# Kernel optimization log

Hardware: AMD Instinct MI355X
Metric: run time of the kernel (lower is better)

The kernel has to match this reference:

```python
import jax, jax.numpy as jnp
import numpy as np
import math

B, NB, HID, KD, NH = 256, 16, 512, 64, 8

def setup_inputs() -> dict:
    key = jax.random.key(0)
    ks = jax.random.split(key, 6)
    s = lambda fan_in: 1.0 / math.sqrt(fan_in)
    return {
        "h": jax.random.normal(ks[0], (B, NB, HID), dtype=jnp.float32),
        "mask": jax.random.randint(ks[1], (B, NB), 0, 2, dtype=jnp.int32),
        "Wk": jax.random.normal(ks[2], (NB, HID, KD * NH), dtype=jnp.float32) * s(HID),
        "Wq": jax.random.normal(ks[3], (NB, HID, KD * NH), dtype=jnp.float32) * s(HID),
        "Wv": jax.random.normal(ks[4], (NB, HID, HID * NH), dtype=jnp.float32) * s(HID),
        "Wo": jax.random.normal(ks[5], (NB, HID * NH, HID), dtype=jnp.float32) * s(HID * NH),
    }

def _group_linear(x, w):
    # x: (B, NB, din), w: (NB, din, dout) -> (B, NB, dout)
    return jnp.einsum('bnd,nde->bne', x, w)

def reference(h, mask, Wk, Wq, Wv, Wo):
    # grouped QKV projections
    k = _group_linear(h, Wk).reshape(B, NB, NH, KD).transpose(0, 2, 1, 3)    # (B,H,NB,KD)
    q = _group_linear(h, Wq).reshape(B, NB, NH, KD).transpose(0, 2, 1, 3)    # (B,H,NB,KD)
    v = _group_linear(h, Wv).reshape(B, NB, NH, HID).transpose(0, 2, 1, 3)   # (B,H,NB,HID)
    scores = jnp.einsum('bhqd,bhkd->bhqk', q, k) / math.sqrt(KD)             # (B,H,NB,NB)
    probs = jax.nn.softmax(scores, axis=-1)
    # post-softmax row mask: mask (B,NB) -> (B,1,NB,1)
    probs = probs * mask.astype(probs.dtype)[:, None, :, None]
    ctx = jnp.einsum('bhqk,bhkd->bhqd', probs, v)                            # (B,H,NB,HID)
    ctx = ctx.transpose(0, 2, 1, 3).reshape(B, NB, NH * HID)                 # (B,NB,H*HID)
    return _group_linear(ctx, Wo)                                            # (B,NB,HID)
```

## Files before the change

kernel.cpp:

```cpp
#include <hip/hip_runtime.h>


typedef short s16x4 __attribute__((ext_vector_type(4)));
typedef short s16x8 __attribute__((ext_vector_type(8)));
typedef float f32x4 __attribute__((ext_vector_type(4)));

__device__ __forceinline__ unsigned short f2bf(float f) {
  unsigned int u = __builtin_bit_cast(unsigned int, f);
  u += 0x7fffu + ((u >> 16) & 1u);
  return (unsigned short)(u >> 16);
}
__device__ __forceinline__ float bf2f(unsigned short s) {
  unsigned int u = ((unsigned int)s) << 16;
  return __builtin_bit_cast(float, u);
}

__global__ __launch_bounds__(256) void qkv_gemm(
    const float* __restrict__ h, const float* __restrict__ Wq,
    const float* __restrict__ Wk, const float* __restrict__ Wv,
    unsigned short* __restrict__ qo, unsigned short* __restrict__ ko,
    unsigned short* __restrict__ vo)
{
  const int g    = blockIdx.y;
  const int m0   = (blockIdx.x / 40) * 128;
  const int n0   = (blockIdx.x % 40) * 128;
  const int tid  = threadIdx.x;
  const int lane = tid & 63;
  const int wave = tid >> 6;
  const int wm   = (wave >> 1) * 64;
  const int wn   = (wave & 1) * 64;

  const float* W; unsigned short* out; int obase, oldc, wN, c0;
  if (n0 < 512)       { W = Wq + (size_t)g * 262144;  out = qo; obase = g * 512;  oldc = 8192;  wN = 512;  c0 = n0; }
  else if (n0 < 1024) { W = Wk + (size_t)g * 262144;  out = ko; obase = g * 512;  oldc = 8192;  wN = 512;  c0 = n0 - 512; }
  else                { W = Wv + (size_t)g * 2097152; out = vo; obase = g * 4096; oldc = 65536; wN = 4096; c0 = n0 - 1024; }

  const float* A = h + (size_t)g * 512 + (size_t)m0 * 8192;

  __shared__ unsigned short As[128][32];
  __shared__ unsigned short Bs[128][36];

  f32x4 acc[4][4];
  #pragma unroll
  for (int i = 0; i < 4; i++)
    #pragma unroll
    for (int j = 0; j < 4; j++) acc[i][j] = (f32x4){0.f, 0.f, 0.f, 0.f};

  const int fr = lane & 15, fq = lane >> 4;

  for (int k0 = 0; k0 < 512; k0 += 32) {
    __syncthreads();
    #pragma unroll
    for (int p = 0; p < 4; p++) {
      int idx = p * 256 + tid;
      int row = idx >> 3, kc = idx & 7;
      float4 av = *reinterpret_cast<const float4*>(A + (size_t)row * 8192 + k0 + kc * 4);
      s16x4 st = { (short)f2bf(av.x), (short)f2bf(av.y), (short)f2bf(av.z), (short)f2bf(av.w) };
      *reinterpret_cast<s16x4*>(&As[row][kc * 4]) = st;
    }
    #pragma unroll
    for (int p = 0; p < 4; p++) {
      int idx = p * 256 + tid;
      int n = idx & 127, kc = idx >> 7;
      const float* wp = W + (size_t)(k0 + kc * 4) * wN + c0 + n;
      float w0 = wp[0], w1 = wp[wN], w2 = wp[2 * wN], w3 = wp[3 * wN];
      s16x4 st = { (short)f2bf(w0), (short)f2bf(w1), (short)f2bf(w2), (short)f2bf(w3) };
      *reinterpret_cast<s16x4*>(&Bs[n][kc * 4]) = st;
    }
    __syncthreads();
    s16x8 af[4], bfr[4];
    #pragma unroll
    for (int mi = 0; mi < 4; mi++)
      af[mi] = *reinterpret_cast<const s16x8*>(&As[wm + mi * 16 + fr][fq * 8]);
    #pragma unroll
    for (int ni = 0; ni < 4; ni++) {
      const s16x4* bp = reinterpret_cast<const s16x4*>(&Bs[wn + ni * 16 + fr][fq * 8]);
      s16x4 lo = bp[0], hi = bp[1];
      bfr[ni] = __builtin_shufflevector(lo, hi, 0, 1, 2, 3, 4, 5, 6, 7);
    }
    #pragma unroll
    for (int mi = 0; mi < 4; mi++)
      #pragma unroll
      for (int ni = 0; ni < 4; ni++)
        acc[mi][ni] = __builtin_amdgcn_mfma_f32_16x16x32_bf16(af[mi], bfr[ni], acc[mi][ni], 0, 0, 0);
  }

  #pragma unroll
  for (int mi = 0; mi < 4; mi++)
    #pragma unroll
    for (int ni = 0; ni < 4; ni++)
      #pragma unroll
      for (int r = 0; r < 4; r++) {
        int row = m0 + wm + mi * 16 + fq * 4 + r;
        int col = c0 + wn + ni * 16 + fr;
        out[(size_t)obase + (size_t)row * oldc + col] = f2bf(acc[mi][ni][r]);
      }
}

__global__ __launch_bounds__(256) void attn_kernel(
    const unsigned short* __restrict__ q, const unsigned short* __restrict__ k,
    const unsigned short* __restrict__ v, const int* __restrict__ mask,
    unsigned short* __restrict__ ctx)
{
  const int b  = blockIdx.x >> 3;
  const int hh = blockIdx.x & 7;
  const int tid = threadIdx.x;

  __shared__ float qs[16][65];
  __shared__ float ks[16][65];
  __shared__ float sc[16][16];

  #pragma unroll
  for (int p = 0; p < 4; p++) {
    int idx = p * 256 + tid;
    int n = idx >> 6, d = idx & 63;
    size_t gi = ((size_t)(b * 16 + n) << 9) + (hh << 6) + d;
    qs[n][d] = bf2f(q[gi]);
    ks[n][d] = bf2f(k[gi]);
  }
  __syncthreads();
  {
    int qi = tid >> 4, ki = tid & 15;
    float s = 0.f;
    #pragma unroll
    for (int j = 0; j < 64; j++) s += qs[qi][j] * ks[ki][j];
    sc[qi][ki] = s * 0.125f;
  }
  __syncthreads();
  if (tid < 16) {
    float m = sc[tid][0];
    #pragma unroll
    for (int j = 1; j < 16; j++) m = fmaxf(m, sc[tid][j]);
    float ev[16], sum = 0.f;
    #pragma unroll
    for (int j = 0; j < 16; j++) { ev[j] = __expf(sc[tid][j] - m); sum += ev[j]; }
    float scale = (mask[b * 16 + tid] != 0) ? (1.f / sum) : 0.f;
    #pragma unroll
    for (int j = 0; j < 16; j++) sc[tid][j] = ev[j] * scale;
  }
  __syncthreads();
  #pragma unroll
  for (int p = 0; p < 2; p++) {
    int e0 = p * 256 + tid;
    float vv[16];
    #pragma unroll
    for (int kk = 0; kk < 16; kk++)
      vv[kk] = bf2f(v[((size_t)(b * 16 + kk) << 12) + (hh << 9) + e0]);
    #pragma unroll
    for (int qi = 0; qi < 16; qi++) {
      float s = 0.f;
      #pragma unroll
      for (int kk = 0; kk < 16; kk++) s += sc[qi][kk] * vv[kk];
      ctx[((size_t)(b * 16 + qi) << 12) + (hh << 9) + e0] = f2bf(s);
    }
  }
}

__global__ __launch_bounds__(256) void out_gemm(
    const unsigned short* __restrict__ ctxp, const float* __restrict__ Wo,
    float* __restrict__ outp)
{
  const int g    = blockIdx.y;
  const int bx   = blockIdx.x;
  const int sk   = bx >> 3;
  const int m0   = ((bx >> 2) & 1) * 128;
  const int n0   = (bx & 3) * 128;
  const int tid  = threadIdx.x;
  const int lane = tid & 63;
  const int wave = tid >> 6;
  const int wm   = (wave >> 1) * 64;
  const int wn   = (wave & 1) * 64;

  const unsigned short* A = ctxp + (size_t)g * 4096 + (size_t)m0 * 65536;
  const float* W = Wo + (size_t)g * 2097152;

  __shared__ unsigned short As[128][32];
  __shared__ unsigned short Bs[128][36];

  f32x4 acc[4][4];
  #pragma unroll
  for (int i = 0; i < 4; i++)
    #pragma unroll
    for (int j = 0; j < 4; j++) acc[i][j] = (f32x4){0.f, 0.f, 0.f, 0.f};

  const int fr = lane & 15, fq = lane >> 4;
  const int kend = sk * 2048 + 2048;

  for (int k0 = sk * 2048; k0 < kend; k0 += 32) {
    __syncthreads();
    #pragma unroll
    for (int p = 0; p < 4; p++) {
      int idx = p * 256 + tid;
      int row = idx >> 3, kc = idx & 7;
      s16x4 av = *reinterpret_cast<const s16x4*>(A + (size_t)row * 65536 + k0 + kc * 4);
      *reinterpret_cast<s16x4*>(&As[row][kc * 4]) = av;
    }
    #pragma unroll
    for (int p = 0; p < 4; p++) {
      int idx = p * 256 + tid;
      int n = idx & 127, kc = idx >> 7;
      const float* wp = W + (size_t)(k0 + kc * 4) * 512 + n0 + n;
      float w0 = wp[0], w1 = wp[512], w2 = wp[1024], w3 = wp[1536];
      s16x4 st = { (short)f2bf(w0), (short)f2bf(w1), (short)f2bf(w2), (short)f2bf(w3) };
      *reinterpret_cast<s16x4*>(&Bs[n][kc * 4]) = st;
    }
    __syncthreads();
    s16x8 af[4], bfr[4];
    #pragma unroll
    for (int mi = 0; mi < 4; mi++)
      af[mi] = *reinterpret_cast<const s16x8*>(&As[wm + mi * 16 + fr][fq * 8]);
    #pragma unroll
    for (int ni = 0; ni < 4; ni++) {
      const s16x4* bp = reinterpret_cast<const s16x4*>(&Bs[wn + ni * 16 + fr][fq * 8]);
      s16x4 lo = bp[0], hi = bp[1];
      bfr[ni] = __builtin_shufflevector(lo, hi, 0, 1, 2, 3, 4, 5, 6, 7);
    }
    #pragma unroll
    for (int mi = 0; mi < 4; mi++)
      #pragma unroll
      for (int ni = 0; ni < 4; ni++)
        acc[mi][ni] = __builtin_amdgcn_mfma_f32_16x16x32_bf16(af[mi], bfr[ni], acc[mi][ni], 0, 0, 0);
  }

  float* og = outp + (size_t)g * 512;
  #pragma unroll
  for (int mi = 0; mi < 4; mi++)
    #pragma unroll
    for (int ni = 0; ni < 4; ni++)
      #pragma unroll
      for (int r = 0; r < 4; r++) {
        int row = m0 + wm + mi * 16 + fq * 4 + r;
        int col = n0 + wn + ni * 16 + fr;
        atomicAdd(&og[(size_t)row * 8192 + col], acc[mi][ni][r]);
      }
}

extern "C" void kernel_launch(void* const* d_in, const int* in_sizes, int n_in,
                              void* d_out, int out_size, void* d_ws, size_t ws_size,
                              hipStream_t stream) {
  const float* h  = (const float*)d_in[0];
  const int* mask = (const int*)d_in[1];
  const float* Wk = (const float*)d_in[2];
  const float* Wq = (const float*)d_in[3];
  const float* Wv = (const float*)d_in[4];
  const float* Wo = (const float*)d_in[5];
  float* out = (float*)d_out;

  unsigned short* qws   = (unsigned short*)d_ws;
  unsigned short* kws   = qws + 2097152;
  unsigned short* vws   = kws + 2097152;
  unsigned short* ctxws = vws + 16777216;

  hipMemsetAsync(d_out, 0, (size_t)out_size * sizeof(float), stream);
  qkv_gemm<<<dim3(80, 16), 256, 0, stream>>>(h, Wq, Wk, Wv, qws, kws, vws);
  attn_kernel<<<2048, 256, 0, stream>>>(qws, kws, vws, mask, ctxws);
  out_gemm<<<dim3(16, 16), 256, 0, stream>>>(ctxws, Wo, out);
}
```

Baseline: 418.6 us.

## Retile GEMMs over full batch, pre-convert h, and replace atomics with split-K reduce

Adds a pass that converts h to bf16 once, so the QKV GEMM loads 16-byte bf16 A tiles. The QKV GEMM is retiled to 256x64, so each block covers the whole batch and each weight tile is read and converted only once. The attention kernel now uses vectorized ushort4 loads and stores, and each thread computes 8 query rows by 4 columns. The output GEMM uses 512-thread blocks with a 4-way split-K that writes partial sums to workspace, followed by a reduce kernel. This removes the memset and the float atomics, at the cost of extra partial-buffer traffic and two more launches.

```diff
diff --git a/kernel.cpp b/kernel.cpp
--- a/kernel.cpp
+++ b/kernel.cpp
@@ -15,202 +15,214 @@
   return __builtin_bit_cast(float, u);
 }
 
+__global__ __launch_bounds__(256) void cvt_h(const float* __restrict__ h,
+                                             unsigned short* __restrict__ hb)
+{
+  int i = (blockIdx.x * 256 + threadIdx.x) * 4;
+  float4 v = *reinterpret_cast<const float4*>(h + i);
+  s16x4 st = { (short)f2bf(v.x), (short)f2bf(v.y), (short)f2bf(v.z), (short)f2bf(v.w) };
+  *reinterpret_cast<s16x4*>(hb + i) = st;
+}
+
 __global__ __launch_bounds__(256) void qkv_gemm(
-    const float* __restrict__ h, const float* __restrict__ Wq,
+    const unsigned short* __restrict__ hb, const float* __restrict__ Wq,
     const float* __restrict__ Wk, const float* __restrict__ Wv,
     unsigned short* __restrict__ qo, unsigned short* __restrict__ ko,
     unsigned short* __restrict__ vo)
 {
   const int g    = blockIdx.y;
-  const int m0   = (blockIdx.x / 40) * 128;
-  const int n0   = (blockIdx.x % 40) * 128;
+  const int n0   = blockIdx.x * 64;
+  const int tid  = threadIdx.x;
+  const int lane = tid & 63;
+  const int wave = tid >> 6;
+  const int wm   = wave * 64;
+
+  const float* W; unsigned short* out; size_t obase; int oldc, wN, c0;
+  if (n0 < 512)       { W = Wq + (size_t)g * 262144;  out = qo; obase = (size_t)g * 512;  oldc = 8192;  wN = 512;  c0 = n0; }
+  else if (n0 < 1024) { W = Wk + (size_t)g * 262144;  out = ko; obase = (size_t)g * 512;  oldc = 8192;  wN = 512;  c0 = n0 - 512; }
+  else                { W = Wv + (size_t)g * 2097152; out = vo; obase = (size_t)g * 4096; oldc = 65536; wN = 4096; c0 = n0 - 1024; }
+
+  const unsigned short* A = hb + (size_t)g * 512;
+
+  __shared__ unsigned short As[256][32];
+  __shared__ unsigned short Bs[64][36];
+
+  f32x4 acc[4][4];
+  #pragma unroll
+  for (int i = 0; i < 4; i++)
+    #pragma unroll
+    for (int j = 0; j < 4; j++) acc[i][j] = (f32x4){0.f, 0.f, 0.f, 0.f};
+
+  const int fr = lane & 15, fq = lane >> 4;
+
+  for (int k0 = 0; k0 < 512; k0 += 32) {
+    __syncthreads();
+    #pragma unroll
+    for (int p = 0; p < 4; p++) {
+      int idx = p * 256 + tid;
+      int row = idx >> 2, kq = idx & 3;
+      *reinterpret_cast<s16x8*>(&As[row][kq * 8]) =
+          *reinterpret_cast<const s16x8*>(A + (size_t)row * 8192 + k0 + kq * 8);
+    }
+    #pragma unroll
+    for (int p = 0; p < 2; p++) {
+      int idx = p * 256 + tid;
+      int n = idx & 63, kc = idx >> 6;
+      const float* wp = W + (size_t)(k0 + kc * 4) * wN + c0 + n;
+      float w0 = wp[0], w1 = wp[wN], w2 = wp[2 * wN], w3 = wp[3 * wN];
+      s16x4 st = { (short)f2bf(w0), (short)f2bf(w1), (short)f2bf(w2), (short)f2bf(w3) };
+      *reinterpret_cast<s16x4*>(&Bs[n][kc * 4]) = st;
+    }
+    __syncthreads();
+    s16x8 af[4], bfr[4];
+    #pragma unroll
+    for (int mi = 0; mi < 4; mi++)
+      af[mi] = *reinterpret_cast<const s16x8*>(&As[wm + mi * 16 + fr][fq * 8]);
+    #pragma unroll
+    for (int ni = 0; ni < 4; ni++) {
+      const s16x4* bp = reinterpret_cast<const s16x4*>(&Bs[ni * 16 + fr][fq * 8]);
+      s16x4 lo = bp[0], hi = bp[1];
+      bfr[ni] = __builtin_shufflevector(lo, hi, 0, 1, 2, 3, 4, 5, 6, 7);
+    }
+    #pragma unroll
+    for (int mi = 0; mi < 4; mi++)
+      #pragma unroll
+      for (int ni = 0; ni < 4; ni++)
+        acc[mi][ni] = __builtin_amdgcn_mfma_f32_16x16x32_bf16(af[mi], bfr[ni], acc[mi][ni], 0, 0, 0);
+  }
+
+  #pragma unroll
+  for (int mi = 0; mi < 4; mi++)
+    #pragma unroll
+    for (int ni = 0; ni < 4; ni++)
+      #pragma unroll
+      for (int r = 0; r < 4; r++) {
+        int row = wm + mi * 16 + fq * 4 + r;
+        int col = c0 + ni * 16 + fr;
+        out[obase + (size_t)row * oldc + col] = f2bf(acc[mi][ni][r]);
+      }
+}
+
+__global__ __launch_bounds__(256) void attn_kernel(
+    const unsigned short* __restrict__ q, const unsigned short* __restrict__ k,
+    const unsigned short* __restrict__ v, const int* __restrict__ mask,
+    unsigned short* __restrict__ ctx)
+{
+  const int b  = blockIdx.x >> 3;
+  const int hh = blockIdx.x & 7;
+  const int tid = threadIdx.x;
+
+  __shared__ float qs[16][65];
+  __shared__ float ks[16][65];
+  __shared__ float sc[16][16];
+
+  {
+    int n = tid >> 4, d4 = (tid & 15) * 4;
+    size_t gi = ((size_t)(b * 16 + n) << 9) + (hh << 6) + d4;
+    ushort4 qv = *reinterpret_cast<const ushort4*>(q + gi);
+    ushort4 kv = *reinterpret_cast<const ushort4*>(k + gi);
+    qs[n][d4] = bf2f(qv.x); qs[n][d4+1] = bf2f(qv.y); qs[n][d4+2] = bf2f(qv.z); qs[n][d4+3] = bf2f(qv.w);
+    ks[n][d4] = bf2f(kv.x); ks[n][d4+1] = bf2f(kv.y); ks[n][d4+2] = bf2f(kv.z); ks[n][d4+3] = bf2f(kv.w);
+  }
+  __syncthreads();
+  {
+    int qi = tid >> 4, ki = tid & 15;
+    float s = 0.f;
+    #pragma unroll
+    for (int j = 0; j < 64; j++) s += qs[qi][j] * ks[ki][j];
+    sc[qi][ki] = s * 0.125f;
+  }
+  __syncthreads();
+  if (tid < 16) {
+    float m = sc[tid][0];
+    #pragma unroll
+    for (int j = 1; j < 16; j++) m = fmaxf(m, sc[tid][j]);
+    float ev[16], sum = 0.f;
+    #pragma unroll
+    for (int j = 0; j < 16; j++) { ev[j] = __expf(sc[tid][j] - m); sum += ev[j]; }
+    float scale = (mask[b * 16 + tid] != 0) ? (1.f / sum) : 0.f;
+    #pragma unroll
+    for (int j = 0; j < 16; j++) sc[tid][j] = ev[j] * scale;
+  }
+  __syncthreads();
+  {
+    int col4  = (tid & 127) * 4;
+    int qbase = (tid >> 7) * 8;
+    float a0[8], a1[8], a2[8], a3[8];
+    #pragma unroll
+    for (int j = 0; j < 8; j++) { a0[j] = 0.f; a1[j] = 0.f; a2[j] = 0.f; a3[j] = 0.f; }
+    #pragma unroll
+    for (int kk = 0; kk < 16; kk++) {
+      ushort4 vv = *reinterpret_cast<const ushort4*>(
+          v + ((size_t)(b * 16 + kk) << 12) + (hh << 9) + col4);
+      float v0 = bf2f(vv.x), v1 = bf2f(vv.y), v2 = bf2f(vv.z), v3 = bf2f(vv.w);
+      #pragma unroll
+      for (int j = 0; j < 8; j++) {
+        float p = sc[qbase + j][kk];
+        a0[j] += p * v0; a1[j] += p * v1; a2[j] += p * v2; a3[j] += p * v3;
+      }
+    }
+    #pragma unroll
+    for (int j = 0; j < 8; j++) {
+      ushort4 st = { f2bf(a0[j]), f2bf(a1[j]), f2bf(a2[j]), f2bf(a3[j]) };
+      *reinterpret_cast<ushort4*>(
+          ctx + ((size_t)(b * 16 + qbase + j) << 12) + (hh << 9) + col4) = st;
+    }
+  }
+}
+
+__global__ __launch_bounds__(512) void out_gemm(
+    const unsigned short* __restrict__ ctxp, const float* __restrict__ Wo,
+    float* __restrict__ partial)
+{
+  const int g    = blockIdx.y;
+  const int bx   = blockIdx.x;
+  const int sk   = bx >> 3;
+  const int n0   = (bx & 7) * 64;
   const int tid  = threadIdx.x;
   const int lane = tid & 63;
   const int wave = tid >> 6;
   const int wm   = (wave >> 1) * 64;
-  const int wn   = (wave & 1) * 64;
-
-  const float* W; unsigned short* out; int obase, oldc, wN, c0;
-  if (n0 < 512)       { W = Wq + (size_t)g * 262144;  out = qo; obase = g * 512;  oldc = 8192;  wN = 512;  c0 = n0; }
-  else if (n0 < 1024) { W = Wk + (size_t)g * 262144;  out = ko; obase = g * 512;  oldc = 8192;  wN = 512;  c0 = n0 - 512; }
-  else                { W = Wv + (size_t)g * 2097152; out = vo; obase = g * 4096; oldc = 65536; wN = 4096; c0 = n0 - 1024; }
-
-  const float* A = h + (size_t)g * 512 + (size_t)m0 * 8192;
-
-  __shared__ unsigned short As[128][32];
-  __shared__ unsigned short Bs[128][36];
-
-  f32x4 acc[4][4];
+  const int wn   = (wave & 1) * 32;
+
+  const unsigned short* A = ctxp + (size_t)g * 4096;
+  const float* W = Wo + (size_t)g * 2097152;
+
+  __shared__ unsigned short As[256][32];
+  __shared__ unsigned short Bs[64][36];
+
+  f32x4 acc[4][2];
   #pragma unroll
   for (int i = 0; i < 4; i++)
     #pragma unroll
-    for (int j = 0; j < 4; j++) acc[i][j] = (f32x4){0.f, 0.f, 0.f, 0.f};
+    for (int j = 0; j < 2; j++) acc[i][j] = (f32x4){0.f, 0.f, 0.f, 0.f};
 
   const int fr = lane & 15, fq = lane >> 4;
-
-  for (int k0 = 0; k0 < 512; k0 += 32) {
-    __syncthreads();
-    #pragma unroll
-    for (int p = 0; p < 4; p++) {
-      int idx = p * 256 + tid;
-      int row = idx >> 3, kc = idx & 7;
-      float4 av = *reinterpret_cast<const float4*>(A + (size_t)row * 8192 + k0 + kc * 4);
-      s16x4 st = { (short)f2bf(av.x), (short)f2bf(av.y), (short)f2bf(av.z), (short)f2bf(av.w) };
-      *reinterpret_cast<s16x4*>(&As[row][kc * 4]) = st;
-    }
-    #pragma unroll
-    for (int p = 0; p < 4; p++) {
-      int idx = p * 256 + tid;
-      int n = idx & 127, kc = idx >> 7;
-      const float* wp = W + (size_t)(k0 + kc * 4) * wN + c0 + n;
-      float w0 = wp[0], w1 = wp[wN], w2 = wp[2 * wN], w3 = wp[3 * wN];
-      s16x4 st = { (short)f2bf(w0), (short)f2bf(w1), (short)f2bf(w2), (short)f2bf(w3) };
-      *reinterpret_cast<s16x4*>(&Bs[n][kc * 4]) = st;
-    }
-    __syncthreads();
-    s16x8 af[4], bfr[4];
-    #pragma unroll
-    for (int mi = 0; mi < 4; mi++)
-      af[mi] = *reinterpret_cast<const s16x8*>(&As[wm + mi * 16 + fr][fq * 8]);
-    #pragma unroll
-    for (int ni = 0; ni < 4; ni++) {
-      const s16x4* bp = reinterpret_cast<const s16x4*>(&Bs[wn + ni * 16 + fr][fq * 8]);
-      s16x4 lo = bp[0], hi = bp[1];
-      bfr[ni] = __builtin_shufflevector(lo, hi, 0, 1, 2, 3, 4, 5, 6, 7);
-    }
-    #pragma unroll
-    for (int mi = 0; mi < 4; mi++)
-      #pragma unroll
-      for (int ni = 0; ni < 4; ni++)
-        acc[mi][ni] = __builtin_amdgcn_mfma_f32_16x16x32_bf16(af[mi], bfr[ni], acc[mi][ni], 0, 0, 0);
-  }
-
-  #pragma unroll
-  for (int mi = 0; mi < 4; mi++)
-    #pragma unroll
-    for (int ni = 0; ni < 4; ni++)
-      #pragma unroll
-      for (int r = 0; r < 4; r++) {
-        int row = m0 + wm + mi * 16 + fq * 4 + r;
-        int col = c0 + wn + ni * 16 + fr;
-        out[(size_t)obase + (size_t)row * oldc + col] = f2bf(acc[mi][ni][r]);
-      }
-}
-
-__global__ __launch_bounds__(256) void attn_kernel(
-    const unsigned short* __restrict__ q, const unsigned short* __restrict__ k,
-    const unsigned short* __restrict__ v, const int* __restrict__ mask,
-    unsigned short* __restrict__ ctx)
-{
-  const int b  = blockIdx.x >> 3;
-  const int hh = blockIdx.x & 7;
-  const int tid = threadIdx.x;
-
-  __shared__ float qs[16][65];
-  __shared__ float ks[16][65];
-  __shared__ float sc[16][16];
-
-  #pragma unroll
-  for (int p = 0; p < 4; p++) {
-    int idx = p * 256 + tid;
-    int n = idx >> 6, d = idx & 63;
-    size_t gi = ((size_t)(b * 16 + n) << 9) + (hh << 6) + d;
-    qs[n][d] = bf2f(q[gi]);
-    ks[n][d] = bf2f(k[gi]);
-  }
-  __syncthreads();
-  {
-    int qi = tid >> 4, ki = tid & 15;
-    float s = 0.f;
-    #pragma unroll
-    for (int j = 0; j < 64; j++) s += qs[qi][j] * ks[ki][j];
-    sc[qi][ki] = s * 0.125f;
-  }
-  __syncthreads();
-  if (tid < 16) {
-    float m = sc[tid][0];
-    #pragma unroll
-    for (int j = 1; j < 16; j++) m = fmaxf(m, sc[tid][j]);
-    float ev[16], sum = 0.f;
-    #pragma unroll
-    for (int j = 0; j < 16; j++) { ev[j] = __expf(sc[tid][j] - m); sum += ev[j]; }
-    float scale = (mask[b * 16 + tid] != 0) ? (1.f / sum) : 0.f;
-    #pragma unroll
-    for (int j = 0; j < 16; j++) sc[tid][j] = ev[j] * scale;
-  }
-  __syncthreads();
-  #pragma unroll
-  for (int p = 0; p < 2; p++) {
-    int e0 = p * 256 + tid;
-    float vv[16];
-    #pragma unroll
-    for (int kk = 0; kk < 16; kk++)
-      vv[kk] = bf2f(v[((size_t)(b * 16 + kk) << 12) + (hh << 9) + e0]);
-    #pragma unroll
-    for (int qi = 0; qi < 16; qi++) {
-      float s = 0.f;
-      #pragma unroll
-      for (int kk = 0; kk < 16; kk++) s += sc[qi][kk] * vv[kk];
-      ctx[((size_t)(b * 16 + qi) << 12) + (hh << 9) + e0] = f2bf(s);
-    }
-  }
-}
-
-__global__ __launch_bounds__(256) void out_gemm(
-    const unsigned short* __restrict__ ctxp, const float* __restrict__ Wo,
-    float* __restrict__ outp)
-{
-  const int g    = blockIdx.y;
-  const int bx   = blockIdx.x;
-  const int sk   = bx >> 3;
-  const int m0   = ((bx >> 2) & 1) * 128;
-  const int n0   = (bx & 3) * 128;
-  const int tid  = threadIdx.x;
-  const int lane = tid & 63;
-  const int wave = tid >> 6;
-  const int wm   = (wave >> 1) * 64;
-  const int wn   = (wave & 1) * 64;
-
-  const unsigned short* A = ctxp + (size_t)g * 4096 + (size_t)m0 * 65536;
-  const float* W = Wo + (size_t)g * 2097152;
-
-  __shared__ unsigned short As[128][32];
-  __shared__ unsigned short Bs[128][36];
-
-  f32x4 acc[4][4];
-  #pragma unroll
-  for (int i = 0; i < 4; i++)
-    #pragma unroll
-    for (int j = 0; j < 4; j++) acc[i][j] = (f32x4){0.f, 0.f, 0.f, 0.f};
-
-  const int fr = lane & 15, fq = lane >> 4;
-  const int kend = sk * 2048 + 2048;
-
-  for (int k0 = sk * 2048; k0 < kend; k0 += 32) {
-    __syncthreads();
-    #pragma unroll
-    for (int p = 0; p < 4; p++) {
-      int idx = p * 256 + tid;
-      int row = idx >> 3, kc = idx & 7;
-      s16x4 av = *reinterpret_cast<const s16x4*>(A + (size_t)row * 65536 + k0 + kc * 4);
-      *reinterpret_cast<s16x4*>(&As[row][kc * 4]) = av;
-    }
-    #pragma unroll
-    for (int p = 0; p < 4; p++) {
-      int idx = p * 256 + tid;
-      int n = idx & 127, kc = idx >> 7;
+  const int kend = sk * 1024 + 1024;
+
+  for (int k0 = sk * 1024; k0 < kend; k0 += 32) {
+    __syncthreads();
+    #pragma unroll
+    for (int p = 0; p < 2; p++) {
+      int idx = p * 512 + tid;
+      int row = idx >> 2, kq = idx & 3;
+      *reinterpret_cast<s16x8*>(&As[row][kq * 8]) =
+          *reinterpret_cast<const s16x8*>(A + (size_t)row * 65536 + k0 + kq * 8);
+    }
+    {
+      int n = tid & 63, kc = tid >> 6;
       const float* wp = W + (size_t)(k0 + kc * 4) * 512 + n0 + n;
       float w0 = wp[0], w1 = wp[512], w2 = wp[1024], w3 = wp[1536];
       s16x4 st = { (short)f2bf(w0), (short)f2bf(w1), (short)f2bf(w2), (short)f2bf(w3) };
       *reinterpret_cast<s16x4*>(&Bs[n][kc * 4]) = st;
     }
     __syncthreads();
-    s16x8 af[4], bfr[4];
+    s16x8 af[4], bfr[2];
     #pragma unroll
     for (int mi = 0; mi < 4; mi++)
       af[mi] = *reinterpret_cast<const s16x8*>(&As[wm + mi * 16 + fr][fq * 8]);
     #pragma unroll
-    for (int ni = 0; ni < 4; ni++) {
+    for (int ni = 0; ni < 2; ni++) {
       const s16x4* bp = reinterpret_cast<const s16x4*>(&Bs[wn + ni * 16 + fr][fq * 8]);
       s16x4 lo = bp[0], hi = bp[1];
       bfr[ni] = __builtin_shufflevector(lo, hi, 0, 1, 2, 3, 4, 5, 6, 7);
@@ -218,21 +230,34 @@
     #pragma unroll
     for (int mi = 0; mi < 4; mi++)
       #pragma unroll
-      for (int ni = 0; ni < 4; ni++)
+      for (int ni = 0; ni < 2; ni++)
         acc[mi][ni] = __builtin_amdgcn_mfma_f32_16x16x32_bf16(af[mi], bfr[ni], acc[mi][ni], 0, 0, 0);
   }
 
-  float* og = outp + (size_t)g * 512;
+  float* pg = partial + (size_t)sk * 2097152 + (size_t)g * 512;
   #pragma unroll
   for (int mi = 0; mi < 4; mi++)
     #pragma unroll
-    for (int ni = 0; ni < 4; ni++)
+    for (int ni = 0; ni < 2; ni++)
       #pragma unroll
       for (int r = 0; r < 4; r++) {
-        int row = m0 + wm + mi * 16 + fq * 4 + r;
+        int row = wm + mi * 16 + fq * 4 + r;
         int col = n0 + wn + ni * 16 + fr;
-        atomicAdd(&og[(size_t)row * 8192 + col], acc[mi][ni][r]);
+        pg[(size_t)row * 8192 + col] = acc[mi][ni][r];
       }
+}
+
+__global__ __launch_bounds__(256) void reduce4(const float* __restrict__ part,
+                                               float* __restrict__ out)
+{
+  int i = (blockIdx.x * 256 + threadIdx.x) * 4;
+  float4 a = *reinterpret_cast<const float4*>(part + i);
+  float4 b = *reinterpret_cast<const float4*>(part + 2097152 + i);
+  float4 c = *reinterpret_cast<const float4*>(part + 4194304 + i);
+  float4 d = *reinterpret_cast<const float4*>(part + 6291456 + i);
+  float4 s = { a.x + b.x + c.x + d.x, a.y + b.y + c.y + d.y,
+               a.z + b.z + c.z + d.z, a.w + b.w + c.w + d.w };
+  *reinterpret_cast<float4*>(out + i) = s;
 }
 
 extern "C" void kernel_launch(void* const* d_in, const int* in_sizes, int n_in,
@@ -250,9 +275,12 @@
   unsigned short* kws   = qws + 2097152;
   unsigned short* vws   = kws + 2097152;
   unsigned short* ctxws = vws + 16777216;
-
-  hipMemsetAsync(d_out, 0, (size_t)out_size * sizeof(float), stream);
-  qkv_gemm<<<dim3(80, 16), 256, 0, stream>>>(h, Wq, Wk, Wv, qws, kws, vws);
+  unsigned short* hb    = ctxws;
+  float* part           = (float*)d_ws;
+
+  cvt_h<<<2048, 256, 0, stream>>>(h, hb);
+  qkv_gemm<<<dim3(80, 16), 256, 0, stream>>>(hb, Wq, Wk, Wv, qws, kws, vws);
   attn_kernel<<<2048, 256, 0, stream>>>(qws, kws, vws, mask, ctxws);
-  out_gemm<<<dim3(16, 16), 256, 0, stream>>>(ctxws, Wo, out);
-}
+  out_gemm<<<dim3(32, 16), 512, 0, stream>>>(ctxws, Wo, part);
+  reduce4<<<2048, 256, 0, stream>>>(part, out);
+}
```

Measured after the change: 388.0 us. 7.3% less time.
